# Kernel tuning notes

Measured on AMD Instinct MI355X. Metric: run time of the kernel, lower is better.

Reference implementation:

```python
import jax, jax.numpy as jnp
import numpy as np

BN_EPS = 1e-5


def setup_inputs() -> dict:
    key = jax.random.key(0)
    ks = jax.random.split(key, 8)
    B, S, D, H, O = 4, 25000, 128, 128, 128
    N, E = B * S, 600000
    x = jax.random.normal(ks[0], (B, S, D), dtype=jnp.float32)
    edge_index = jax.random.randint(ks[1], (2, E), 0, N)
    W1 = jax.random.normal(ks[2], (D, H), dtype=jnp.float32) * (1.0 / np.sqrt(D))
    b1 = jnp.zeros((H,), jnp.float32)
    gamma1 = jnp.ones((H,), jnp.float32)
    beta1 = jnp.zeros((H,), jnp.float32)
    W2 = jax.random.normal(ks[3], (H, O), dtype=jnp.float32) * (1.0 / np.sqrt(H))
    b2 = jnp.zeros((O,), jnp.float32)
    return {"x": x, "edge_index": edge_index, "W1": W1, "b1": b1,
            "gamma1": gamma1, "beta1": beta1, "W2": W2, "b2": b2}


def _gcn_norm(edge_index, num_nodes, dtype):
    # PyG gcn_norm: add self-loops, symmetric D^-1/2 (A+I) D^-1/2 edge weights.
    row, col = edge_index
    loop = jnp.arange(num_nodes, dtype=row.dtype)
    row_f = jnp.concatenate([row, loop])
    col_f = jnp.concatenate([col, loop])
    deg = jax.ops.segment_sum(jnp.ones(row_f.shape, dtype), row_f,
                              num_segments=num_nodes)
    dis = jnp.where(deg > 0, jax.lax.rsqrt(jnp.maximum(deg, 1e-12)), 0.0)
    norm = dis[row_f] * dis[col_f]  # [E + N]
    return row_f, col_f, norm


def _gcn_conv(h, W, b, row_f, col_f, norm, num_nodes):
    hw = h @ W                       # [N, out]
    msg = hw[col_f] * norm[:, None]  # gather + scale, [E+N, out]
    out = jax.ops.segment_sum(msg, row_f, num_segments=num_nodes)
    return out + b


def reference(x, edge_index, W1, b1, gamma1, beta1, W2, b2):
    B, S, D = x.shape
    N = B * S
    h = x.reshape(N, D)
    row_f, col_f, norm = _gcn_norm(edge_index, N, h.dtype)
    # layer 1: GCNConv -> BatchNorm (batch stats) -> ReLU (dropout inactive in eval)
    h = _gcn_conv(h, W1, b1, row_f, col_f, norm, N)
    mean = jnp.mean(h, axis=0)
    var = jnp.mean(jnp.square(h - mean), axis=0)
    h = gamma1 * (h - mean) * jax.lax.rsqrt(var + BN_EPS) + beta1
    h = jax.nn.relu(h)
    # layer 2: final GCNConv
    h = _gcn_conv(h, W2, b2, row_f, col_f, norm, N)
    return h.reshape(B, S, -1)
```

## Files before the change

### kernel.cpp

```cpp
#include <hip/hip_runtime.h>

#define DIM 128
#define BN_EPS 1e-5f

typedef short short8 __attribute__((ext_vector_type(8)));
typedef float floatx4 __attribute__((ext_vector_type(4)));

__device__ __forceinline__ unsigned short f2bf(float f) {
    unsigned int u = __builtin_bit_cast(unsigned int, f);
    u += 0x7FFFu + ((u >> 16) & 1u);
    return (unsigned short)(u >> 16);
}
__device__ __forceinline__ float bf2f(unsigned short h) {
    return __builtin_bit_cast(float, (unsigned int)h << 16);
}


__global__ void deg_kernel(const int* __restrict__ row, int* __restrict__ deg, int E) {
    int e = blockIdx.x * blockDim.x + threadIdx.x;
    if (e < E) atomicAdd(&deg[row[e]], 1);
}

__global__ void dis_kernel(const int* __restrict__ deg, float* __restrict__ dis, int n) {
    int i = blockIdx.x * blockDim.x + threadIdx.x;
    if (i < n) dis[i] = rsqrtf((float)(deg[i] + 1));
}


__global__ __launch_bounds__(256) void scan_block_kernel(const int* __restrict__ deg,
                                                         int* __restrict__ rowptr,
                                                         int* __restrict__ aux, int n) {
    __shared__ int ls[256];
    const int base = blockIdx.x * 1024;
    const int t = threadIdx.x;
    int v[4]; int s = 0;
    #pragma unroll
    for (int k = 0; k < 4; ++k) {
        int i = base + t * 4 + k;
        v[k] = (i < n) ? deg[i] : 0;
        s += v[k];
    }
    ls[t] = s;
    __syncthreads();
    for (int off = 1; off < 256; off <<= 1) {
        int x = (t >= off) ? ls[t - off] : 0;
        __syncthreads();
        ls[t] += x;
        __syncthreads();
    }
    int excl = ls[t] - s;
    if (t == 255) aux[blockIdx.x] = ls[255];
    #pragma unroll
    for (int k = 0; k < 4; ++k) {
        int i = base + t * 4 + k;
        if (i < n) rowptr[i] = excl;
        excl += v[k];
    }
}

__global__ void scan_aux_kernel(int* __restrict__ aux, int nb, int* __restrict__ rowptr, int n, int E) {
    int s = 0;
    for (int i = 0; i < nb; ++i) { int v = aux[i]; aux[i] = s; s += v; }
    rowptr[n] = E;
}

__global__ void add_offsets_kernel(int* __restrict__ rowptr, const int* __restrict__ aux, int n) {
    int i = blockIdx.x * blockDim.x + threadIdx.x;
    if (i < n) rowptr[i] += aux[i >> 10];
}


__global__ void scatter_kernel(const int* __restrict__ row, const int* __restrict__ col,
                               const float* __restrict__ dis, const int* __restrict__ rowptr,
                               int* __restrict__ cursor, int2* __restrict__ epack, int E) {
    int e = blockIdx.x * blockDim.x + threadIdx.x;
    if (e >= E) return;
    int r = row[e], c = col[e];
    int pos = rowptr[r] + atomicAdd(&cursor[r], 1);
    float nrm = dis[r] * dis[c];
    epack[pos] = make_int2(c, __builtin_bit_cast(int, nrm));
}


__global__ void convert_w_kernel(const float* __restrict__ W1, const float* __restrict__ W2,
                                 unsigned short* __restrict__ wfrag) {
    int s = blockIdx.x * blockDim.x + threadIdx.x;
    if (s >= 4096) return;
    int m  = s >> 11;
    int s2 = s & 2047;
    int kt = s2 >> 9;
    int nt = (s2 >> 6) & 7;
    int l  = s2 & 63;
    const float* W = m ? W2 : W1;
    unsigned short* o = wfrag + (size_t)m * 16384 + (size_t)s2 * 8;
    int k0 = kt * 32 + (l >> 4) * 8;
    int n0 = nt * 16 + (l & 15);
    #pragma unroll
    for (int j = 0; j < 8; ++j) o[j] = f2bf(W[(k0 + j) * DIM + n0]);
}


__global__ __launch_bounds__(256) void gemm_mfma_f32_kernel(
    const float* __restrict__ A, const unsigned short* __restrict__ wfrag,
    unsigned short* __restrict__ C, int n)
{
    __shared__ unsigned short sA[64][136];
    const int tid  = threadIdx.x;
    const int row0 = blockIdx.x * 64;

    #pragma unroll
    for (int l = 0; l < 8; ++l) {
        int idx = tid + l * 256;
        int r   = idx >> 5;
        int c4  = (idx & 31) * 4;
        float4 v;
        if (row0 + r < n) v = *(const float4*)(A + (size_t)(row0 + r) * DIM + c4);
        else              v = make_float4(0.f, 0.f, 0.f, 0.f);
        unsigned int lo = (unsigned int)f2bf(v.x) | ((unsigned int)f2bf(v.y) << 16);
        unsigned int hi = (unsigned int)f2bf(v.z) | ((unsigned int)f2bf(v.w) << 16);
        *(uint2*)(&sA[r][c4]) = make_uint2(lo, hi);
    }
    __syncthreads();

    const int wave = tid >> 6;
    const int lane = tid & 63;
    const int m    = lane & 15;
    const int quad = lane >> 4;
    const int rowA = wave * 16 + m;

    short8 af[4];
    #pragma unroll
    for (int kt = 0; kt < 4; ++kt)
        af[kt] = *(const short8*)(&sA[rowA][kt * 32 + quad * 8]);

    floatx4 acc[8];
    #pragma unroll
    for (int nt = 0; nt < 8; ++nt) acc[nt] = (floatx4){0.f, 0.f, 0.f, 0.f};

    #pragma unroll
    for (int nt = 0; nt < 8; ++nt)
        #pragma unroll
        for (int kt = 0; kt < 4; ++kt) {
            short8 bfr = *(const short8*)(wfrag + ((size_t)(kt * 8 + nt) * 64 + lane) * 8);
            acc[nt] = __builtin_amdgcn_mfma_f32_16x16x32_bf16(af[kt], bfr, acc[nt], 0, 0, 0);
        }

    #pragma unroll
    for (int nt = 0; nt < 8; ++nt)
        #pragma unroll
        for (int r = 0; r < 4; ++r) {
            int rr = row0 + wave * 16 + quad * 4 + r;
            if (rr < n) C[(size_t)rr * DIM + nt * 16 + m] = f2bf(acc[nt][r]);
        }
}


__global__ __launch_bounds__(256) void gemm_mfma_bn_kernel(
    const unsigned short* __restrict__ A, const unsigned short* __restrict__ wfrag,
    unsigned short* __restrict__ C, int n,
    const float* __restrict__ mean, const float* __restrict__ istd,
    const float* __restrict__ gamma, const float* __restrict__ beta)
{
    __shared__ unsigned short sA[64][136];
    const int tid  = threadIdx.x;
    const int row0 = blockIdx.x * 64;

    #pragma unroll
    for (int l = 0; l < 4; ++l) {
        int idx = tid + l * 256;
        int r   = idx >> 4;
        int c8  = (idx & 15) * 8;
        uint4 u = make_uint4(0, 0, 0, 0);
        if (row0 + r < n) u = *(const uint4*)(A + (size_t)(row0 + r) * DIM + c8);
        float f[8] = { bf2f((unsigned short)(u.x & 0xffff)), bf2f((unsigned short)(u.x >> 16)),
                       bf2f((unsigned short)(u.y & 0xffff)), bf2f((unsigned short)(u.y >> 16)),
                       bf2f((unsigned short)(u.z & 0xffff)), bf2f((unsigned short)(u.z >> 16)),
                       bf2f((unsigned short)(u.w & 0xffff)), bf2f((unsigned short)(u.w >> 16)) };
        #pragma unroll
        for (int k = 0; k < 8; ++k) {
            int c = c8 + k;
            f[k] = fmaxf(fmaf(gamma[c] * (f[k] - mean[c]), istd[c], beta[c]), 0.f);
        }
        uint4 o;
        o.x = (unsigned int)f2bf(f[0]) | ((unsigned int)f2bf(f[1]) << 16);
        o.y = (unsigned int)f2bf(f[2]) | ((unsigned int)f2bf(f[3]) << 16);
        o.z = (unsigned int)f2bf(f[4]) | ((unsigned int)f2bf(f[5]) << 16);
        o.w = (unsigned int)f2bf(f[6]) | ((unsigned int)f2bf(f[7]) << 16);
        *(uint4*)(&sA[r][c8]) = o;
    }
    __syncthreads();

    const int wave = tid >> 6;
    const int lane = tid & 63;
    const int m    = lane & 15;
    const int quad = lane >> 4;
    const int rowA = wave * 16 + m;

    short8 af[4];
    #pragma unroll
    for (int kt = 0; kt < 4; ++kt)
        af[kt] = *(const short8*)(&sA[rowA][kt * 32 + quad * 8]);

    floatx4 acc[8];
    #pragma unroll
    for (int nt = 0; nt < 8; ++nt) acc[nt] = (floatx4){0.f, 0.f, 0.f, 0.f};

    #pragma unroll
    for (int nt = 0; nt < 8; ++nt)
        #pragma unroll
        for (int kt = 0; kt < 4; ++kt) {
            short8 bfr = *(const short8*)(wfrag + ((size_t)(kt * 8 + nt) * 64 + lane) * 8);
            acc[nt] = __builtin_amdgcn_mfma_f32_16x16x32_bf16(af[kt], bfr, acc[nt], 0, 0, 0);
        }

    #pragma unroll
    for (int nt = 0; nt < 8; ++nt)
        #pragma unroll
        for (int r = 0; r < 4; ++r) {
            int rr = row0 + wave * 16 + quad * 4 + r;
            if (rr < n) C[(size_t)rr * DIM + nt * 16 + m] = f2bf(acc[nt][r]);
        }
}


template <bool OUT_BF16>
__global__ __launch_bounds__(256) void agg_csr_kernel(
    const unsigned short* __restrict__ hw, const float* __restrict__ dis,
    const int* __restrict__ rowptr, const int2* __restrict__ epack,
    const float* __restrict__ bias, void* __restrict__ out_, int n)
{
    const int sub  = threadIdx.x >> 4;
    const int l    = threadIdx.x & 15;
    const int node = blockIdx.x * 16 + sub;
    if (node >= n) return;
    const int j = l * 8;

    float acc[8];
    {
        const float d = dis[node];
        const float dd = d * d;
        uint4 u = *(const uint4*)(hw + (size_t)node * DIM + j);
        unsigned int uu[4] = {u.x, u.y, u.z, u.w};
        #pragma unroll
        for (int k = 0; k < 4; ++k) {
            acc[2*k]   = bf2f((unsigned short)(uu[k] & 0xffff)) * dd;
            acc[2*k+1] = bf2f((unsigned short)(uu[k] >> 16))    * dd;
        }
    }

    int p  = rowptr[node];
    const int pe = rowptr[node + 1];
    for (; p + 1 < pe; p += 2) {
        int2 e0 = epack[p], e1 = epack[p + 1];
        float w0 = __builtin_bit_cast(float, e0.y);
        float w1 = __builtin_bit_cast(float, e1.y);
        uint4 u0 = *(const uint4*)(hw + (size_t)e0.x * DIM + j);
        uint4 u1 = *(const uint4*)(hw + (size_t)e1.x * DIM + j);
        unsigned int a[4] = {u0.x, u0.y, u0.z, u0.w};
        unsigned int b[4] = {u1.x, u1.y, u1.z, u1.w};
        #pragma unroll
        for (int k = 0; k < 4; ++k) {
            acc[2*k]   = fmaf(bf2f((unsigned short)(a[k] & 0xffff)), w0, acc[2*k]);
            acc[2*k+1] = fmaf(bf2f((unsigned short)(a[k] >> 16)),    w0, acc[2*k+1]);
            acc[2*k]   = fmaf(bf2f((unsigned short)(b[k] & 0xffff)), w1, acc[2*k]);
            acc[2*k+1] = fmaf(bf2f((unsigned short)(b[k] >> 16)),    w1, acc[2*k+1]);
        }
    }
    if (p < pe) {
        int2 e = epack[p];
        float w = __builtin_bit_cast(float, e.y);
        uint4 u = *(const uint4*)(hw + (size_t)e.x * DIM + j);
        unsigned int a[4] = {u.x, u.y, u.z, u.w};
        #pragma unroll
        for (int k = 0; k < 4; ++k) {
            acc[2*k]   = fmaf(bf2f((unsigned short)(a[k] & 0xffff)), w, acc[2*k]);
            acc[2*k+1] = fmaf(bf2f((unsigned short)(a[k] >> 16)),    w, acc[2*k+1]);
        }
    }

    float4 b0 = *(const float4*)(bias + j);
    float4 b1 = *(const float4*)(bias + j + 4);
    acc[0] += b0.x; acc[1] += b0.y; acc[2] += b0.z; acc[3] += b0.w;
    acc[4] += b1.x; acc[5] += b1.y; acc[6] += b1.z; acc[7] += b1.w;

    if (OUT_BF16) {
        unsigned short* out = (unsigned short*)out_;
        uint4 o;
        o.x = (unsigned int)f2bf(acc[0]) | ((unsigned int)f2bf(acc[1]) << 16);
        o.y = (unsigned int)f2bf(acc[2]) | ((unsigned int)f2bf(acc[3]) << 16);
        o.z = (unsigned int)f2bf(acc[4]) | ((unsigned int)f2bf(acc[5]) << 16);
        o.w = (unsigned int)f2bf(acc[6]) | ((unsigned int)f2bf(acc[7]) << 16);
        *(uint4*)(out + (size_t)node * DIM + j) = o;
    } else {
        float* out = (float*)out_;
        *(float4*)(out + (size_t)node * DIM + j)     = make_float4(acc[0], acc[1], acc[2], acc[3]);
        *(float4*)(out + (size_t)node * DIM + j + 4) = make_float4(acc[4], acc[5], acc[6], acc[7]);
    }
}


__global__ __launch_bounds__(256) void stats_kernel(const unsigned short* __restrict__ h,
                                                    float* __restrict__ stat, int n)
{
    const int tid = threadIdx.x;
    const int cg  = tid & 15;
    const int rg  = tid >> 4;
    float s[8], q[8];
    #pragma unroll
    for (int k = 0; k < 8; ++k) { s[k] = 0.f; q[k] = 0.f; }

    const int stride = gridDim.x * 16;
    for (int i = blockIdx.x * 16 + rg; i < n; i += 2 * stride) {
        uint4 u0 = *(const uint4*)(h + (size_t)i * DIM + cg * 8);
        int i1 = i + stride;
        uint4 u1 = (i1 < n) ? *(const uint4*)(h + (size_t)i1 * DIM + cg * 8)
                            : make_uint4(0, 0, 0, 0);
        unsigned int a[4] = {u0.x, u0.y, u0.z, u0.w};
        unsigned int b[4] = {u1.x, u1.y, u1.z, u1.w};
        #pragma unroll
        for (int k = 0; k < 4; ++k) {
            float a0 = bf2f((unsigned short)(a[k] & 0xffff));
            float a1 = bf2f((unsigned short)(a[k] >> 16));
            float c0 = bf2f((unsigned short)(b[k] & 0xffff));
            float c1 = bf2f((unsigned short)(b[k] >> 16));
            s[2*k]   += a0 + c0;
            s[2*k+1] += a1 + c1;
            q[2*k]   = fmaf(a0, a0, fmaf(c0, c0, q[2*k]));
            q[2*k+1] = fmaf(a1, a1, fmaf(c1, c1, q[2*k+1]));
        }
    }

    __shared__ float red[16][128];
    #pragma unroll
    for (int k = 0; k < 8; ++k) red[rg][cg * 8 + k] = s[k];
    __syncthreads();
    if (tid < 128) {
        float t = 0.f;
        #pragma unroll
        for (int r = 0; r < 16; ++r) t += red[r][tid];
        atomicAdd(&stat[tid], t);
    }
    __syncthreads();
    #pragma unroll
    for (int k = 0; k < 8; ++k) red[rg][cg * 8 + k] = q[k];
    __syncthreads();
    if (tid < 128) {
        float t = 0.f;
        #pragma unroll
        for (int r = 0; r < 16; ++r) t += red[r][tid];
        atomicAdd(&stat[DIM + tid], t);
    }
}

__global__ void bn_finalize_kernel(const float* __restrict__ stat, float* __restrict__ mi, int n) {
    int j = threadIdx.x;
    if (j < DIM) {
        float mean = stat[j] / (float)n;
        float var  = stat[DIM + j] / (float)n - mean * mean;
        mi[j]       = mean;
        mi[DIM + j] = rsqrtf(var + BN_EPS);
    }
}


extern "C" void kernel_launch(void* const* d_in, const int* in_sizes, int n_in,
                              void* d_out, int out_size, void* d_ws, size_t ws_size,
                              hipStream_t stream)
{
    const float* x      = (const float*)d_in[0];
    const int*   ei     = (const int*)  d_in[1];
    const float* W1     = (const float*)d_in[2];
    const float* b1     = (const float*)d_in[3];
    const float* gamma1 = (const float*)d_in[4];
    const float* beta1  = (const float*)d_in[5];
    const float* W2     = (const float*)d_in[6];
    const float* b2     = (const float*)d_in[7];
    float* out = (float*)d_out;

    const int N = in_sizes[0] / DIM;
    const int E = in_sizes[1] / 2;
    const int* row = ei;
    const int* col = ei + E;

    const int NB = (N + 1023) / 1024;

    unsigned short* hw    = (unsigned short*)d_ws;
    unsigned short* h1    = hw + (size_t)N * DIM;
    int2*  epack  = (int2*)(h1 + (size_t)N * DIM);
    unsigned short* wfrag = (unsigned short*)(epack + E);
    float* dis    = (float*)(wfrag + 2 * 16384);
    int*   deg    = (int*)(dis + N);
    int*   cursor = deg + N;
    int*   rowptr = cursor + N;
    int*   aux    = rowptr + N + 1;
    float* stat   = (float*)(aux + 128);
    float* mi     = stat + 256;

    hipMemsetAsync(deg,    0, (size_t)N * sizeof(int), stream);
    hipMemsetAsync(cursor, 0, (size_t)N * sizeof(int), stream);
    hipMemsetAsync(stat,   0, 256 * sizeof(float), stream);

    deg_kernel<<<(E + 255) / 256, 256, 0, stream>>>(row, deg, E);
    dis_kernel<<<(N + 255) / 256, 256, 0, stream>>>(deg, dis, N);
    scan_block_kernel<<<NB, 256, 0, stream>>>(deg, rowptr, aux, N);
    scan_aux_kernel<<<1, 1, 0, stream>>>(aux, NB, rowptr, N, E);
    add_offsets_kernel<<<(N + 255) / 256, 256, 0, stream>>>(rowptr, aux, N);
    scatter_kernel<<<(E + 255) / 256, 256, 0, stream>>>(row, col, dis, rowptr, cursor,
                                                        epack, E);
    convert_w_kernel<<<16, 256, 0, stream>>>(W1, W2, wfrag);

    gemm_mfma_f32_kernel<<<(N + 63) / 64, 256, 0, stream>>>(x, wfrag, hw, N);
    agg_csr_kernel<true><<<(N + 15) / 16, 256, 0, stream>>>(hw, dis, rowptr, epack, b1, h1, N);
    stats_kernel<<<512, 256, 0, stream>>>(h1, stat, N);
    bn_finalize_kernel<<<1, DIM, 0, stream>>>(stat, mi, N);

    gemm_mfma_bn_kernel<<<(N + 63) / 64, 256, 0, stream>>>(h1, wfrag + 16384, hw, N,
                                                           mi, mi + DIM, gamma1, beta1);
    agg_csr_kernel<false><<<(N + 15) / 16, 256, 0, stream>>>(hw, dis, rowptr, epack, b2, out, N);
}
```

Before: 315.4 us.

## Fuse BN statistics into aggregation, parallelize aux scan, and unroll gather loop

Computes the BatchNorm sum and sum-of-squares inside the first CSR aggregation kernel instead of a separate stats pass, removing one full read of the hidden activations. The degree-normalization computation is folded into the block scan, and the single-thread aux scan becomes a 256-thread parallel scan. The cursor is initialized from rowptr to drop a memset, and the edge gather loop is unrolled by four for more memory-level parallelism. The trade-off is many more per-block float atomics on the same 256 stat addresses, and statistics taken from fp32 values rather than rounded bf16.

Result: slower. 463.2 us (+46.9%).

```diff
diff --git a/kernel.cpp b/kernel.cpp
--- a/kernel.cpp
+++ b/kernel.cpp
@@ -21,15 +21,11 @@
     if (e < E) atomicAdd(&deg[row[e]], 1);
 }
 
-__global__ void dis_kernel(const int* __restrict__ deg, float* __restrict__ dis, int n) {
-    int i = blockIdx.x * blockDim.x + threadIdx.x;
-    if (i < n) dis[i] = rsqrtf((float)(deg[i] + 1));
-}
-
 
 __global__ __launch_bounds__(256) void scan_block_kernel(const int* __restrict__ deg,
                                                          int* __restrict__ rowptr,
-                                                         int* __restrict__ aux, int n) {
+                                                         int* __restrict__ aux,
+                                                         float* __restrict__ dis, int n) {
     __shared__ int ls[256];
     const int base = blockIdx.x * 1024;
     const int t = threadIdx.x;
@@ -53,30 +49,49 @@
     #pragma unroll
     for (int k = 0; k < 4; ++k) {
         int i = base + t * 4 + k;
-        if (i < n) rowptr[i] = excl;
+        if (i < n) {
+            rowptr[i] = excl;
+            dis[i] = rsqrtf((float)(v[k] + 1));
+        }
         excl += v[k];
     }
 }
 
-__global__ void scan_aux_kernel(int* __restrict__ aux, int nb, int* __restrict__ rowptr, int n, int E) {
-    int s = 0;
-    for (int i = 0; i < nb; ++i) { int v = aux[i]; aux[i] = s; s += v; }
-    rowptr[n] = E;
-}
-
-__global__ void add_offsets_kernel(int* __restrict__ rowptr, const int* __restrict__ aux, int n) {
+__global__ __launch_bounds__(256) void scan_aux_kernel(int* __restrict__ aux, int nb,
+                                                       int* __restrict__ rowptr, int n, int E) {
+    __shared__ int ls[256];
+    const int t = threadIdx.x;
+    int v = (t < nb) ? aux[t] : 0;
+    ls[t] = v;
+    __syncthreads();
+    for (int off = 1; off < 256; off <<= 1) {
+        int x = (t >= off) ? ls[t - off] : 0;
+        __syncthreads();
+        ls[t] += x;
+        __syncthreads();
+    }
+    if (t < nb) aux[t] = ls[t] - v;
+    if (t == 0) rowptr[n] = E;
+}
+
+__global__ void add_offsets_kernel(int* __restrict__ rowptr, int* __restrict__ cursor,
+                                   const int* __restrict__ aux, int n) {
     int i = blockIdx.x * blockDim.x + threadIdx.x;
-    if (i < n) rowptr[i] += aux[i >> 10];
+    if (i < n) {
+        int v = rowptr[i] + aux[i >> 10];
+        rowptr[i] = v;
+        cursor[i] = v;
+    }
 }
 
 
 __global__ void scatter_kernel(const int* __restrict__ row, const int* __restrict__ col,
-                               const float* __restrict__ dis, const int* __restrict__ rowptr,
-                               int* __restrict__ cursor, int2* __restrict__ epack, int E) {
+                               const float* __restrict__ dis, int* __restrict__ cursor,
+                               int2* __restrict__ epack, int E) {
     int e = blockIdx.x * blockDim.x + threadIdx.x;
     if (e >= E) return;
     int r = row[e], c = col[e];
-    int pos = rowptr[r] + atomicAdd(&cursor[r], 1);
+    int pos = atomicAdd(&cursor[r], 1);
     float nrm = dis[r] * dis[c];
     epack[pos] = make_int2(c, __builtin_bit_cast(int, nrm));
 }
@@ -223,132 +238,108 @@
 }
 
 
-template <bool OUT_BF16>
+__device__ __forceinline__ void acc8(float* acc, uint4 u, float w) {
+    unsigned int a[4] = {u.x, u.y, u.z, u.w};
+    #pragma unroll
+    for (int k = 0; k < 4; ++k) {
+        acc[2*k]   = fmaf(bf2f((unsigned short)(a[k] & 0xffff)), w, acc[2*k]);
+        acc[2*k+1] = fmaf(bf2f((unsigned short)(a[k] >> 16)),    w, acc[2*k+1]);
+    }
+}
+
+template <bool OUT_BF16, bool STATS>
 __global__ __launch_bounds__(256) void agg_csr_kernel(
     const unsigned short* __restrict__ hw, const float* __restrict__ dis,
     const int* __restrict__ rowptr, const int2* __restrict__ epack,
-    const float* __restrict__ bias, void* __restrict__ out_, int n)
+    const float* __restrict__ bias, void* __restrict__ out_, int n,
+    float* __restrict__ stat)
 {
     const int sub  = threadIdx.x >> 4;
     const int l    = threadIdx.x & 15;
     const int node = blockIdx.x * 16 + sub;
-    if (node >= n) return;
+    const bool valid = node < n;
     const int j = l * 8;
 
     float acc[8];
-    {
-        const float d = dis[node];
-        const float dd = d * d;
-        uint4 u = *(const uint4*)(hw + (size_t)node * DIM + j);
-        unsigned int uu[4] = {u.x, u.y, u.z, u.w};
-        #pragma unroll
-        for (int k = 0; k < 4; ++k) {
-            acc[2*k]   = bf2f((unsigned short)(uu[k] & 0xffff)) * dd;
-            acc[2*k+1] = bf2f((unsigned short)(uu[k] >> 16))    * dd;
-        }
-    }
-
-    int p  = rowptr[node];
-    const int pe = rowptr[node + 1];
-    for (; p + 1 < pe; p += 2) {
-        int2 e0 = epack[p], e1 = epack[p + 1];
-        float w0 = __builtin_bit_cast(float, e0.y);
-        float w1 = __builtin_bit_cast(float, e1.y);
-        uint4 u0 = *(const uint4*)(hw + (size_t)e0.x * DIM + j);
-        uint4 u1 = *(const uint4*)(hw + (size_t)e1.x * DIM + j);
-        unsigned int a[4] = {u0.x, u0.y, u0.z, u0.w};
-        unsigned int b[4] = {u1.x, u1.y, u1.z, u1.w};
-        #pragma unroll
-        for (int k = 0; k < 4; ++k) {
-            acc[2*k]   = fmaf(bf2f((unsigned short)(a[k] & 0xffff)), w0, acc[2*k]);
-            acc[2*k+1] = fmaf(bf2f((unsigned short)(a[k] >> 16)),    w0, acc[2*k+1]);
-            acc[2*k]   = fmaf(bf2f((unsigned short)(b[k] & 0xffff)), w1, acc[2*k]);
-            acc[2*k+1] = fmaf(bf2f((unsigned short)(b[k] >> 16)),    w1, acc[2*k+1]);
-        }
-    }
-    if (p < pe) {
-        int2 e = epack[p];
-        float w = __builtin_bit_cast(float, e.y);
-        uint4 u = *(const uint4*)(hw + (size_t)e.x * DIM + j);
-        unsigned int a[4] = {u.x, u.y, u.z, u.w};
-        #pragma unroll
-        for (int k = 0; k < 4; ++k) {
-            acc[2*k]   = fmaf(bf2f((unsigned short)(a[k] & 0xffff)), w, acc[2*k]);
-            acc[2*k+1] = fmaf(bf2f((unsigned short)(a[k] >> 16)),    w, acc[2*k+1]);
-        }
-    }
-
-    float4 b0 = *(const float4*)(bias + j);
-    float4 b1 = *(const float4*)(bias + j + 4);
-    acc[0] += b0.x; acc[1] += b0.y; acc[2] += b0.z; acc[3] += b0.w;
-    acc[4] += b1.x; acc[5] += b1.y; acc[6] += b1.z; acc[7] += b1.w;
-
-    if (OUT_BF16) {
-        unsigned short* out = (unsigned short*)out_;
-        uint4 o;
-        o.x = (unsigned int)f2bf(acc[0]) | ((unsigned int)f2bf(acc[1]) << 16);
-        o.y = (unsigned int)f2bf(acc[2]) | ((unsigned int)f2bf(acc[3]) << 16);
-        o.z = (unsigned int)f2bf(acc[4]) | ((unsigned int)f2bf(acc[5]) << 16);
-        o.w = (unsigned int)f2bf(acc[6]) | ((unsigned int)f2bf(acc[7]) << 16);
-        *(uint4*)(out + (size_t)node * DIM + j) = o;
-    } else {
-        float* out = (float*)out_;
-        *(float4*)(out + (size_t)node * DIM + j)     = make_float4(acc[0], acc[1], acc[2], acc[3]);
-        *(float4*)(out + (size_t)node * DIM + j + 4) = make_float4(acc[4], acc[5], acc[6], acc[7]);
-    }
-}
-
-
-__global__ __launch_bounds__(256) void stats_kernel(const unsigned short* __restrict__ h,
-                                                    float* __restrict__ stat, int n)
-{
-    const int tid = threadIdx.x;
-    const int cg  = tid & 15;
-    const int rg  = tid >> 4;
-    float s[8], q[8];
-    #pragma unroll
-    for (int k = 0; k < 8; ++k) { s[k] = 0.f; q[k] = 0.f; }
-
-    const int stride = gridDim.x * 16;
-    for (int i = blockIdx.x * 16 + rg; i < n; i += 2 * stride) {
-        uint4 u0 = *(const uint4*)(h + (size_t)i * DIM + cg * 8);
-        int i1 = i + stride;
-        uint4 u1 = (i1 < n) ? *(const uint4*)(h + (size_t)i1 * DIM + cg * 8)
-                            : make_uint4(0, 0, 0, 0);
-        unsigned int a[4] = {u0.x, u0.y, u0.z, u0.w};
-        unsigned int b[4] = {u1.x, u1.y, u1.z, u1.w};
-        #pragma unroll
-        for (int k = 0; k < 4; ++k) {
-            float a0 = bf2f((unsigned short)(a[k] & 0xffff));
-            float a1 = bf2f((unsigned short)(a[k] >> 16));
-            float c0 = bf2f((unsigned short)(b[k] & 0xffff));
-            float c1 = bf2f((unsigned short)(b[k] >> 16));
-            s[2*k]   += a0 + c0;
-            s[2*k+1] += a1 + c1;
-            q[2*k]   = fmaf(a0, a0, fmaf(c0, c0, q[2*k]));
-            q[2*k+1] = fmaf(a1, a1, fmaf(c1, c1, q[2*k+1]));
-        }
-    }
-
-    __shared__ float red[16][128];
-    #pragma unroll
-    for (int k = 0; k < 8; ++k) red[rg][cg * 8 + k] = s[k];
-    __syncthreads();
-    if (tid < 128) {
-        float t = 0.f;
-        #pragma unroll
-        for (int r = 0; r < 16; ++r) t += red[r][tid];
-        atomicAdd(&stat[tid], t);
-    }
-    __syncthreads();
-    #pragma unroll
-    for (int k = 0; k < 8; ++k) red[rg][cg * 8 + k] = q[k];
-    __syncthreads();
-    if (tid < 128) {
-        float t = 0.f;
-        #pragma unroll
-        for (int r = 0; r < 16; ++r) t += red[r][tid];
-        atomicAdd(&stat[DIM + tid], t);
+    #pragma unroll
+    for (int k = 0; k < 8; ++k) acc[k] = 0.f;
+
+    if (valid) {
+        {
+            const float d = dis[node];
+            uint4 u = *(const uint4*)(hw + (size_t)node * DIM + j);
+            acc8(acc, u, d * d);
+        }
+
+        int p  = rowptr[node];
+        const int pe = rowptr[node + 1];
+        for (; p + 3 < pe; p += 4) {
+            int2 e0 = epack[p],     e1 = epack[p + 1];
+            int2 e2 = epack[p + 2], e3 = epack[p + 3];
+            uint4 u0 = *(const uint4*)(hw + (size_t)e0.x * DIM + j);
+            uint4 u1 = *(const uint4*)(hw + (size_t)e1.x * DIM + j);
+            uint4 u2 = *(const uint4*)(hw + (size_t)e2.x * DIM + j);
+            uint4 u3 = *(const uint4*)(hw + (size_t)e3.x * DIM + j);
+            acc8(acc, u0, __builtin_bit_cast(float, e0.y));
+            acc8(acc, u1, __builtin_bit_cast(float, e1.y));
+            acc8(acc, u2, __builtin_bit_cast(float, e2.y));
+            acc8(acc, u3, __builtin_bit_cast(float, e3.y));
+        }
+        if (p + 1 < pe) {
+            int2 e0 = epack[p], e1 = epack[p + 1];
+            uint4 u0 = *(const uint4*)(hw + (size_t)e0.x * DIM + j);
+            uint4 u1 = *(const uint4*)(hw + (size_t)e1.x * DIM + j);
+            acc8(acc, u0, __builtin_bit_cast(float, e0.y));
+            acc8(acc, u1, __builtin_bit_cast(float, e1.y));
+            p += 2;
+        }
+        if (p < pe) {
+            int2 e = epack[p];
+            uint4 u = *(const uint4*)(hw + (size_t)e.x * DIM + j);
+            acc8(acc, u, __builtin_bit_cast(float, e.y));
+        }
+
+        float4 b0 = *(const float4*)(bias + j);
+        float4 b1 = *(const float4*)(bias + j + 4);
+        acc[0] += b0.x; acc[1] += b0.y; acc[2] += b0.z; acc[3] += b0.w;
+        acc[4] += b1.x; acc[5] += b1.y; acc[6] += b1.z; acc[7] += b1.w;
+
+        if (OUT_BF16) {
+            unsigned short* out = (unsigned short*)out_;
+            uint4 o;
+            o.x = (unsigned int)f2bf(acc[0]) | ((unsigned int)f2bf(acc[1]) << 16);
+            o.y = (unsigned int)f2bf(acc[2]) | ((unsigned int)f2bf(acc[3]) << 16);
+            o.z = (unsigned int)f2bf(acc[4]) | ((unsigned int)f2bf(acc[5]) << 16);
+            o.w = (unsigned int)f2bf(acc[6]) | ((unsigned int)f2bf(acc[7]) << 16);
+            *(uint4*)(out + (size_t)node * DIM + j) = o;
+        } else {
+            float* out = (float*)out_;
+            *(float4*)(out + (size_t)node * DIM + j)     = make_float4(acc[0], acc[1], acc[2], acc[3]);
+            *(float4*)(out + (size_t)node * DIM + j + 4) = make_float4(acc[4], acc[5], acc[6], acc[7]);
+        }
+    }
+
+    if constexpr (STATS) {
+        __shared__ float red[16][128];
+        #pragma unroll
+        for (int k = 0; k < 8; ++k) red[sub][j + k] = valid ? acc[k] : 0.f;
+        __syncthreads();
+        if (threadIdx.x < 128) {
+            float t = 0.f;
+            #pragma unroll
+            for (int r = 0; r < 16; ++r) t += red[r][threadIdx.x];
+            atomicAdd(&stat[threadIdx.x], t);
+        }
+        __syncthreads();
+        #pragma unroll
+        for (int k = 0; k < 8; ++k) red[sub][j + k] = valid ? acc[k] * acc[k] : 0.f;
+        __syncthreads();
+        if (threadIdx.x < 128) {
+            float t = 0.f;
+            #pragma unroll
+            for (int r = 0; r < 16; ++r) t += red[r][threadIdx.x];
+            atomicAdd(&stat[DIM + threadIdx.x], t);
+        }
     }
 }
 
@@ -393,28 +384,26 @@
     int*   cursor = deg + N;
     int*   rowptr = cursor + N;
     int*   aux    = rowptr + N + 1;
-    float* stat   = (float*)(aux + 128);
+    float* stat   = (float*)(aux + 256);
     float* mi     = stat + 256;
 
-    hipMemsetAsync(deg,    0, (size_t)N * sizeof(int), stream);
-    hipMemsetAsync(cursor, 0, (size_t)N * sizeof(int), stream);
-    hipMemsetAsync(stat,   0, 256 * sizeof(float), stream);
+    hipMemsetAsync(deg,  0, (size_t)N * sizeof(int), stream);
+    hipMemsetAsync(stat, 0, 256 * sizeof(float), stream);
 
     deg_kernel<<<(E + 255) / 256, 256, 0, stream>>>(row, deg, E);
-    dis_kernel<<<(N + 255) / 256, 256, 0, stream>>>(deg, dis, N);
-    scan_block_kernel<<<NB, 256, 0, stream>>>(deg, rowptr, aux, N);
-    scan_aux_kernel<<<1, 1, 0, stream>>>(aux, NB, rowptr, N, E);
-    add_offsets_kernel<<<(N + 255) / 256, 256, 0, stream>>>(rowptr, aux, N);
-    scatter_kernel<<<(E + 255) / 256, 256, 0, stream>>>(row, col, dis, rowptr, cursor,
-                                                        epack, E);
+    scan_block_kernel<<<NB, 256, 0, stream>>>(deg, rowptr, aux, dis, N);
+    scan_aux_kernel<<<1, 256, 0, stream>>>(aux, NB, rowptr, N, E);
+    add_offsets_kernel<<<(N + 255) / 256, 256, 0, stream>>>(rowptr, cursor, aux, N);
+    scatter_kernel<<<(E + 255) / 256, 256, 0, stream>>>(row, col, dis, cursor, epack, E);
     convert_w_kernel<<<16, 256, 0, stream>>>(W1, W2, wfrag);
 
     gemm_mfma_f32_kernel<<<(N + 63) / 64, 256, 0, stream>>>(x, wfrag, hw, N);
-    agg_csr_kernel<true><<<(N + 15) / 16, 256, 0, stream>>>(hw, dis, rowptr, epack, b1, h1, N);
-    stats_kernel<<<512, 256, 0, stream>>>(h1, stat, N);
+    agg_csr_kernel<true, true><<<(N + 15) / 16, 256, 0, stream>>>(hw, dis, rowptr, epack,
+                                                                  b1, h1, N, stat);
     bn_finalize_kernel<<<1, DIM, 0, stream>>>(stat, mi, N);
 
     gemm_mfma_bn_kernel<<<(N + 63) / 64, 256, 0, stream>>>(h1, wfrag + 16384, hw, N,
                                                            mi, mi + DIM, gamma1, beta1);
-    agg_csr_kernel<false><<<(N + 15) / 16, 256, 0, stream>>>(hw, dis, rowptr, epack, b2, out, N);
-}
+    agg_csr_kernel<false, false><<<(N + 15) / 16, 256, 0, stream>>>(hw, dis, rowptr, epack,
+                                                                    b2, out, N, nullptr);
+}
```
